# Kernel optimization log

Measured on AMD Instinct MI355X. Metric: run time of the kernel, lower is better.

Reference implementation:

```python
import jax, jax.numpy as jnp
import numpy as np

D_MODEL = 1024
N_HEADS = 16
HEAD_DIM = D_MODEL // N_HEADS


def setup_inputs() -> dict:
    key = jax.random.key(0)
    ks = jax.random.split(key, 5)
    T, B = 2048, 2
    x = jax.random.normal(ks[0], (T, B, D_MODEL), dtype=jnp.float32)
    s = 1.0 / np.sqrt(D_MODEL)
    Wq = jax.random.normal(ks[1], (D_MODEL, D_MODEL), dtype=jnp.float32) * s
    Wk = jax.random.normal(ks[2], (D_MODEL, D_MODEL), dtype=jnp.float32) * s
    Wv = jax.random.normal(ks[3], (D_MODEL, D_MODEL), dtype=jnp.float32) * s
    Wo = jax.random.normal(ks[4], (D_MODEL, D_MODEL), dtype=jnp.float32) * s
    return {"x": x, "Wq": Wq, "Wk": Wk, "Wv": Wv, "Wo": Wo}


def reference(x, Wq, Wk, Wv, Wo):
    T, B, C = x.shape
    H, D = N_HEADS, HEAD_DIM

    def split_heads(t):
        # (T,B,C) -> (B,H,T,D), matching view+permute(1,2,0,3)
        return t.reshape(T, B, H, D).transpose(1, 2, 0, 3)

    q = split_heads(x @ Wq.T)
    k = split_heads(x @ Wk.T)
    v = split_heads(x @ Wv.T)

    scale = 1.0 / jnp.sqrt(jnp.asarray(D, dtype=x.dtype))
    scores = jnp.einsum('bhqd,bhkd->bhqk', q, k) * scale  # (B,H,T,T)
    causal = jnp.tril(jnp.ones((T, T), dtype=bool))
    scores = jnp.where(causal, scores, jnp.asarray(-jnp.inf, dtype=scores.dtype))
    probs = jax.nn.softmax(scores, axis=-1)
    ctx = jnp.einsum('bhqk,bhkd->bhqd', probs, v)  # (B,H,T,D)
    ctx = ctx.transpose(2, 0, 1, 3).reshape(T, B, C)
    return ctx @ Wo.T
```

## Files before the change

### kernel.cpp

```cpp
#include <hip/hip_runtime.h>
#include <hip/hip_bf16.h>

#define TT 2048
#define BB 2
#define CC 1024
#define HH 16
#define DD 64
#define MM (TT * BB)

typedef short bf16x8 __attribute__((ext_vector_type(8)));
typedef float f32x4  __attribute__((ext_vector_type(4)));

__device__ inline ushort f2b(float f) {
    union { float f; unsigned u; } v; v.f = f;
    unsigned r = v.u + 0x7FFFu + ((v.u >> 16) & 1u);
    return (ushort)(r >> 16);
}

__device__ inline unsigned pack_bf16(float a, float b) {
    __hip_bfloat162 h = __float22bfloat162_rn(make_float2(a, b));
    union { __hip_bfloat162 h; unsigned u; } c; c.h = h;
    return c.u;
}

__device__ inline void gload_lds16(const ushort* g, ushort* l) {
    __builtin_amdgcn_global_load_lds(
        (const __attribute__((address_space(1))) void*)g,
        (__attribute__((address_space(3))) void*)l, 16, 0, 0);
}

#define XQUADS (MM * CC / 4)
#define WQUADS (CC * CC / 4)
__global__ __launch_bounds__(256) void conv_all(const float* __restrict__ x,
                                                const float* __restrict__ Wq,
                                                const float* __restrict__ Wk,
                                                const float* __restrict__ Wv,
                                                const float* __restrict__ Wo,
                                                ushort* __restrict__ dst) {
    int idx = blockIdx.x * 256 + threadIdx.x;
    const float* src;
    int off;
    if (idx < XQUADS) {
        src = x; off = idx;
    } else {
        int wi = (idx - XQUADS) >> 18;
        off = (idx - XQUADS) & (WQUADS - 1);
        src = (wi == 0) ? Wq : (wi == 1) ? Wk : (wi == 2) ? Wv : Wo;
    }
    float4 v = ((const float4*)src)[off];
    ushort4 o = {f2b(v.x), f2b(v.y), f2b(v.z), f2b(v.w)};
    ((ushort4*)dst)[idx] = o;
}

__global__ __launch_bounds__(256) void gemm_qkv(const ushort* __restrict__ A,
                                                const ushort* __restrict__ B0,
                                                const ushort* __restrict__ B1,
                                                const ushort* __restrict__ B2,
                                                ushort* __restrict__ Oq,
                                                ushort* __restrict__ Ok,
                                                ushort* __restrict__ Ov) {
    __shared__ __align__(16) ushort As[128 * 32];
    __shared__ __align__(16) ushort Bs[128 * 32];

    const int tid = threadIdx.x;
    const int wave = tid >> 6, lane = tid & 63;
    const int quad = lane >> 4, l16 = lane & 15;
    const int wm = wave >> 1, wn = wave & 1;

    const int bm = blockIdx.x * 128;
    const int by = blockIdx.y;
    const int wsel = by >> 3;
    const ushort* Bp = (wsel == 0) ? B0 : (wsel == 1) ? B1 : B2;
    const int bn = (by & 7) * 128;

    const int srow = lane >> 2;
    const int scol = (lane & 3) * 8;

    f32x4 acc[4][4];
#pragma unroll
    for (int i = 0; i < 4; i++)
#pragma unroll
        for (int j = 0; j < 4; j++) acc[i][j] = (f32x4){0.f, 0.f, 0.f, 0.f};

    for (int k0 = 0; k0 < CC; k0 += 32) {
#pragma unroll
        for (int i = 0; i < 2; i++) {
            const int rbase = wave * 32 + i * 16;
            gload_lds16(A + (size_t)(bm + rbase + srow) * CC + k0 + scol,
                        As + rbase * 32);
            gload_lds16(Bp + (size_t)(bn + rbase + srow) * CC + k0 + scol,
                        Bs + rbase * 32);
        }
        __syncthreads();

        bf16x8 af[4], bf[4];
#pragma unroll
        for (int mi = 0; mi < 4; mi++)
            af[mi] = *(const bf16x8*)(As + (wm * 64 + mi * 16 + l16) * 32 + quad * 8);
#pragma unroll
        for (int ni = 0; ni < 4; ni++)
            bf[ni] = *(const bf16x8*)(Bs + (wn * 64 + ni * 16 + l16) * 32 + quad * 8);
#pragma unroll
        for (int mi = 0; mi < 4; mi++)
#pragma unroll
            for (int ni = 0; ni < 4; ni++)
                acc[mi][ni] = __builtin_amdgcn_mfma_f32_16x16x32_bf16(
                    af[mi], bf[ni], acc[mi][ni], 0, 0, 0);
        __syncthreads();
    }

#pragma unroll
    for (int mi = 0; mi < 4; mi++) {
#pragma unroll
        for (int r = 0; r < 4; r++) {
            const int m = bm + wm * 64 + mi * 16 + quad * 4 + r;
#pragma unroll
            for (int ni = 0; ni < 4; ni++) {
                const int colg = bn + wn * 64 + ni * 16 + l16;
                float v = acc[mi][ni][r];
                if (wsel == 0) v *= 0.18033688f;
                const int t = m >> 1, b = m & 1;
                const int h = colg >> 6, d = colg & 63;
                ushort* dst = (wsel == 0) ? Oq : (wsel == 1) ? Ok : Ov;
                dst[(((size_t)(b * HH + h)) * TT + t) * DD + d] = f2b(v);
            }
        }
    }
}

__global__ __launch_bounds__(256) void gemm_out(const ushort* __restrict__ A,
                                                const ushort* __restrict__ Bm,
                                                float* __restrict__ Of) {
    __shared__ __align__(16) ushort As[128 * 32];
    __shared__ __align__(16) ushort Bs[64 * 32];

    const int tid = threadIdx.x;
    const int wave = tid >> 6, lane = tid & 63;
    const int quad = lane >> 4, l16 = lane & 15;

    const int bm = blockIdx.x * 128;
    const int bn = blockIdx.y * 64;

    const int srow = lane >> 2;
    const int scol = (lane & 3) * 8;

    f32x4 acc[2][4];
#pragma unroll
    for (int i = 0; i < 2; i++)
#pragma unroll
        for (int j = 0; j < 4; j++) acc[i][j] = (f32x4){0.f, 0.f, 0.f, 0.f};

    for (int k0 = 0; k0 < CC; k0 += 32) {
#pragma unroll
        for (int i = 0; i < 2; i++) {
            const int rbase = wave * 32 + i * 16;
            gload_lds16(A + (size_t)(bm + rbase + srow) * CC + k0 + scol,
                        As + rbase * 32);
        }
        gload_lds16(Bm + (size_t)(bn + wave * 16 + srow) * CC + k0 + scol,
                    Bs + wave * 16 * 32);
        __syncthreads();

        bf16x8 af[2], bf[4];
#pragma unroll
        for (int mi = 0; mi < 2; mi++)
            af[mi] = *(const bf16x8*)(As + (wave * 32 + mi * 16 + l16) * 32 + quad * 8);
#pragma unroll
        for (int ni = 0; ni < 4; ni++)
            bf[ni] = *(const bf16x8*)(Bs + (ni * 16 + l16) * 32 + quad * 8);
#pragma unroll
        for (int mi = 0; mi < 2; mi++)
#pragma unroll
            for (int ni = 0; ni < 4; ni++)
                acc[mi][ni] = __builtin_amdgcn_mfma_f32_16x16x32_bf16(
                    af[mi], bf[ni], acc[mi][ni], 0, 0, 0);
        __syncthreads();
    }

#pragma unroll
    for (int mi = 0; mi < 2; mi++)
#pragma unroll
        for (int r = 0; r < 4; r++) {
            const int m = bm + wave * 32 + mi * 16 + quad * 4 + r;
#pragma unroll
            for (int ni = 0; ni < 4; ni++)
                Of[(size_t)m * CC + bn + ni * 16 + l16] = acc[mi][ni][r];
        }
}

__global__ __launch_bounds__(256) void prep_kv(const ushort* __restrict__ Kb,
                                               const ushort* __restrict__ Vb,
                                               ushort* __restrict__ Kf,
                                               ushort* __restrict__ Vf) {
    __shared__ __align__(16) ushort Ls[64 * 72];
    const int tile = blockIdx.x;
    const int bh   = blockIdx.y;
    const int t    = threadIdx.x;
    const size_t src = (size_t)bh * TT * DD + (size_t)tile * 64 * DD;
    const size_t dst = (size_t)bh * TT * DD + (size_t)tile * 4096;

#pragma unroll
    for (int i = 0; i < 2; i++) {
        int e = t + i * 256;
        int r = e >> 3, kc = (e & 7) * 8;
        *(uint4*)(Ls + r * 72 + kc) = *(const uint4*)(Kb + src + r * 64 + kc);
    }
    __syncthreads();
#pragma unroll
    for (int i = 0; i < 2; i++) {
        int o = t + i * 256;
        int c = o >> 8, nb = (o >> 6) & 3, lane = o & 63;
        int quad = lane >> 4, l16 = lane & 15;
        int j = nb * 16 + l16, k0 = c * 32 + quad * 8;
        *(uint4*)(Kf + dst + (size_t)o * 8) = *(const uint4*)(Ls + j * 72 + k0);
    }
    __syncthreads();

#pragma unroll
    for (int i = 0; i < 2; i++) {
        int e = t + i * 256;
        int r = e >> 3, kc = (e & 7) * 8;
        *(uint4*)(Ls + r * 72 + kc) = *(const uint4*)(Vb + src + r * 64 + kc);
    }
    __syncthreads();
#pragma unroll
    for (int i = 0; i < 2; i++) {
        int o = t + i * 256;
        int c = o >> 8, db = (o >> 6) & 3, lane = o & 63;
        int quad = lane >> 4, l16 = lane & 15;
        int d = db * 16 + l16;
        ushort tmp[8];
#pragma unroll
        for (int u = 0; u < 8; u++) {
            int jp = c * 32 + quad * 8 + u;
            int j = (jp & 3) * 16 + (jp >> 2);
            tmp[u] = Ls[j * 72 + d];
        }
        *(uint4*)(Vf + dst + (size_t)o * 8) = *(uint4*)tmp;
    }
}

template <bool DIAG>
__device__ __forceinline__ void attn_step(const bf16x8* qa, f32x4* O, float* l,
                                          const bf16x8* kf, const bf16x8* vf,
                                          ushort* P, int j0, int qbase,
                                          int quad, int l16) {
    f32x4 S[4];
#pragma unroll
    for (int nb = 0; nb < 4; nb++) S[nb] = (f32x4){0.f, 0.f, 0.f, 0.f};
#pragma unroll
    for (int c = 0; c < 2; c++)
#pragma unroll
        for (int nb = 0; nb < 4; nb++)
            S[nb] = __builtin_amdgcn_mfma_f32_16x16x32_bf16(qa[c], kf[c * 4 + nb],
                                                            S[nb], 0, 0, 0);

#pragma unroll
    for (int r = 0; r < 4; r++) {
        const int qg = qbase + quad * 4 + r;
        float p[4];
#pragma unroll
        for (int nb = 0; nb < 4; nb++) {
            float s = S[nb][r];
            if (DIAG) { if (j0 + nb * 16 + l16 > qg) s = -1e30f; }
            p[nb] = __builtin_amdgcn_exp2f(s);
        }
        l[r] += (p[0] + p[1]) + (p[2] + p[3]);
        uint2 w; w.x = pack_bf16(p[0], p[1]); w.y = pack_bf16(p[2], p[3]);
        *(uint2*)(P + (quad * 4 + r) * 72 + l16 * 4) = w;
    }

#pragma unroll
    for (int c = 0; c < 2; c++) {
        bf16x8 pa = *(const bf16x8*)(P + l16 * 72 + c * 32 + quad * 8);
#pragma unroll
        for (int db = 0; db < 4; db++)
            O[db] = __builtin_amdgcn_mfma_f32_16x16x32_bf16(pa, vf[c * 4 + db],
                                                            O[db], 0, 0, 0);
    }
}

__global__ __launch_bounds__(256, 2) void attn_mfma(const ushort* __restrict__ Qb,
                                                    const ushort* __restrict__ Kf,
                                                    const ushort* __restrict__ Vf,
                                                    ushort* __restrict__ ctx) {
    __shared__ __align__(16) ushort PsA[4 * 16 * 72];
    __shared__ __align__(16) ushort PsB[4 * 16 * 72];

    const int tid  = threadIdx.x;
    const int wave = tid >> 6;
    const int lane = tid & 63;
    const int quad = lane >> 4;
    const int l16  = lane & 15;

    const int p  = blockIdx.x;
    const int bh = blockIdx.y;
    const int qtA = p, qtB = (TT / 64 - 1) - p;
    const int q0A = qtA * 64 + wave * 16;
    const int q0B = qtB * 64 + wave * 16;

    const size_t baseQK = (size_t)bh * TT * DD;

    bf16x8 qaA[2], qaB[2];
    {
        const ushort* qp = Qb + baseQK + (size_t)(q0A + l16) * DD + quad * 8;
        qaA[0] = *(const bf16x8*)(qp);
        qaA[1] = *(const bf16x8*)(qp + 32);
        const ushort* qp2 = Qb + baseQK + (size_t)(q0B + l16) * DD + quad * 8;
        qaB[0] = *(const bf16x8*)(qp2);
        qaB[1] = *(const bf16x8*)(qp2 + 32);
    }

    f32x4 OA[4], OB[4];
#pragma unroll
    for (int i = 0; i < 4; i++) {
        OA[i] = (f32x4){0.f, 0.f, 0.f, 0.f};
        OB[i] = (f32x4){0.f, 0.f, 0.f, 0.f};
    }
    float lA[4] = {0.f, 0.f, 0.f, 0.f};
    float lB[4] = {0.f, 0.f, 0.f, 0.f};

    ushort* PA = PsA + wave * 16 * 72;
    ushort* PB = PsB + wave * 16 * 72;

    const ushort* Kfp = Kf + baseQK;
    const ushort* Vfp = Vf + baseQK;

    for (int kt = 0; kt <= qtB; kt++) {
        const int j0 = kt * 64;

        bf16x8 kf[8], vf[8];
#pragma unroll
        for (int i = 0; i < 8; i++) {
            kf[i] = *(const bf16x8*)(Kfp + (i << 9) + lane * 8);
            vf[i] = *(const bf16x8*)(Vfp + (i << 9) + lane * 8);
        }

        if (kt == qtB)
            attn_step<true >(qaB, OB, lB, kf, vf, PB, j0, q0B, quad, l16);
        else
            attn_step<false>(qaB, OB, lB, kf, vf, PB, j0, q0B, quad, l16);

        if (kt < qtA)
            attn_step<false>(qaA, OA, lA, kf, vf, PA, j0, q0A, quad, l16);
        else if (kt == qtA)
            attn_step<true >(qaA, OA, lA, kf, vf, PA, j0, q0A, quad, l16);

        Kfp += 4096;
        Vfp += 4096;
    }

    const int b = bh >> 4, h = bh & 15;
#pragma unroll
    for (int r = 0; r < 4; r++) {
        float la = lA[r], lb = lB[r];
        la += __shfl_xor(la, 1); la += __shfl_xor(la, 2);
        la += __shfl_xor(la, 4); la += __shfl_xor(la, 8);
        lb += __shfl_xor(lb, 1); lb += __shfl_xor(lb, 2);
        lb += __shfl_xor(lb, 4); lb += __shfl_xor(lb, 8);
        const float invA = 1.f / la;
        const float invB = 1.f / lb;
        const int tA = q0A + quad * 4 + r;
        const int tB = q0B + quad * 4 + r;
#pragma unroll
        for (int db = 0; db < 4; db++) {
            ctx[((size_t)tA * BB + b) * CC + h * DD + db * 16 + l16] =
                f2b(OA[db][r] * invA);
            ctx[((size_t)tB * BB + b) * CC + h * DD + db * 16 + l16] =
                f2b(OB[db][r] * invB);
        }
    }
}

extern "C" void kernel_launch(void* const* d_in, const int* in_sizes, int n_in,
                              void* d_out, int out_size, void* d_ws, size_t ws_size,
                              hipStream_t stream) {
    const float* x  = (const float*)d_in[0];
    const float* Wq = (const float*)d_in[1];
    const float* Wk = (const float*)d_in[2];
    const float* Wv = (const float*)d_in[3];
    const float* Wo = (const float*)d_in[4];
    float* out = (float*)d_out;

    ushort* xb  = (ushort*)d_ws;
    ushort* Wb  = xb + (size_t)MM * CC;
    ushort* Wqb = Wb;
    ushort* Wkb = Wb + (size_t)CC * CC;
    ushort* Wvb = Wb + 2 * (size_t)CC * CC;
    ushort* Wob = Wb + 3 * (size_t)CC * CC;
    ushort* Qb  = Wb + 4 * (size_t)CC * CC;
    ushort* Kb  = Qb + (size_t)MM * CC;
    ushort* Vb  = Kb + (size_t)MM * CC;
    ushort* Kf  = Vb + (size_t)MM * CC;
    ushort* Vf  = Kf + (size_t)MM * CC;
    ushort* Ctxb = Vf + (size_t)MM * CC;

    conv_all<<<dim3((XQUADS + 4 * WQUADS) / 256), 256, 0, stream>>>(
        x, Wq, Wk, Wv, Wo, xb);

    gemm_qkv<<<dim3(MM / 128, 24), 256, 0, stream>>>(
        xb, Wqb, Wkb, Wvb, Qb, Kb, Vb);

    prep_kv<<<dim3(TT / 64, BB * HH), 256, 0, stream>>>(Kb, Vb, Kf, Vf);

    attn_mfma<<<dim3(TT / 128, BB * HH), 256, 0, stream>>>(Qb, Kf, Vf, Ctxb);

    gemm_out<<<dim3(MM / 128, CC / 64), 256, 0, stream>>>(Ctxb, Wob, out);
}
```

Baseline: 176.2 us.

## Write K in attention fragment layout from QKV GEMM and prefetch K/V tiles

The QKV GEMM epilogue now writes K straight into the MFMA-fragment layout that the attention kernel consumes. This removes the K half of the separate prep kernel, leaving a V-only prep_v, and saves one intermediate buffer plus a read/write pass. The attention loop also loads the next K/V tile into registers while the current tile is computed, to hide global-load latency. The extra register buffers may raise VGPR pressure and lower occupancy.

```diff
diff --git a/kernel.cpp b/kernel.cpp
--- a/kernel.cpp
+++ b/kernel.cpp
@@ -118,11 +118,21 @@
             for (int ni = 0; ni < 4; ni++) {
                 const int colg = bn + wn * 64 + ni * 16 + l16;
                 float v = acc[mi][ni][r];
-                if (wsel == 0) v *= 0.18033688f;
                 const int t = m >> 1, b = m & 1;
                 const int h = colg >> 6, d = colg & 63;
-                ushort* dst = (wsel == 0) ? Oq : (wsel == 1) ? Ok : Ov;
-                dst[(((size_t)(b * HH + h)) * TT + t) * DD + d] = f2b(v);
+                if (wsel == 0) {
+                    v *= 0.18033688f;
+                    Oq[(((size_t)(b * HH + h)) * TT + t) * DD + d] = f2b(v);
+                } else if (wsel == 1) {
+                    const int jj = t & 63;
+                    size_t idx = ((size_t)(b * HH + h) * TT) * DD
+                               + (size_t)(t >> 6) * 4096
+                               + (d >> 5) * 2048 + (jj >> 4) * 512
+                               + (((d >> 3) & 3) * 16 + (jj & 15)) * 8 + (d & 7);
+                    Ok[idx] = f2b(v);
+                } else {
+                    Ov[(((size_t)(b * HH + h)) * TT + t) * DD + d] = f2b(v);
+                }
             }
         }
     }
@@ -188,33 +198,14 @@
         }
 }
 
-__global__ __launch_bounds__(256) void prep_kv(const ushort* __restrict__ Kb,
-                                               const ushort* __restrict__ Vb,
-                                               ushort* __restrict__ Kf,
-                                               ushort* __restrict__ Vf) {
+__global__ __launch_bounds__(256) void prep_v(const ushort* __restrict__ Vb,
+                                              ushort* __restrict__ Vf) {
     __shared__ __align__(16) ushort Ls[64 * 72];
     const int tile = blockIdx.x;
     const int bh   = blockIdx.y;
     const int t    = threadIdx.x;
     const size_t src = (size_t)bh * TT * DD + (size_t)tile * 64 * DD;
     const size_t dst = (size_t)bh * TT * DD + (size_t)tile * 4096;
-
-#pragma unroll
-    for (int i = 0; i < 2; i++) {
-        int e = t + i * 256;
-        int r = e >> 3, kc = (e & 7) * 8;
-        *(uint4*)(Ls + r * 72 + kc) = *(const uint4*)(Kb + src + r * 64 + kc);
-    }
-    __syncthreads();
-#pragma unroll
-    for (int i = 0; i < 2; i++) {
-        int o = t + i * 256;
-        int c = o >> 8, nb = (o >> 6) & 3, lane = o & 63;
-        int quad = lane >> 4, l16 = lane & 15;
-        int j = nb * 16 + l16, k0 = c * 32 + quad * 8;
-        *(uint4*)(Kf + dst + (size_t)o * 8) = *(const uint4*)(Ls + j * 72 + k0);
-    }
-    __syncthreads();
 
 #pragma unroll
     for (int i = 0; i < 2; i++) {
@@ -326,14 +317,24 @@
     const ushort* Kfp = Kf + baseQK;
     const ushort* Vfp = Vf + baseQK;
 
+    bf16x8 kf[8], vf[8], kn[8], vn[8];
+#pragma unroll
+    for (int i = 0; i < 8; i++) {
+        kf[i] = *(const bf16x8*)(Kfp + (i << 9) + lane * 8);
+        vf[i] = *(const bf16x8*)(Vfp + (i << 9) + lane * 8);
+    }
+
     for (int kt = 0; kt <= qtB; kt++) {
         const int j0 = kt * 64;
 
-        bf16x8 kf[8], vf[8];
-#pragma unroll
-        for (int i = 0; i < 8; i++) {
-            kf[i] = *(const bf16x8*)(Kfp + (i << 9) + lane * 8);
-            vf[i] = *(const bf16x8*)(Vfp + (i << 9) + lane * 8);
+        if (kt < qtB) {
+            const ushort* Kn = Kfp + (((size_t)kt + 1) << 12);
+            const ushort* Vn = Vfp + (((size_t)kt + 1) << 12);
+#pragma unroll
+            for (int i = 0; i < 8; i++) {
+                kn[i] = *(const bf16x8*)(Kn + (i << 9) + lane * 8);
+                vn[i] = *(const bf16x8*)(Vn + (i << 9) + lane * 8);
+            }
         }
 
         if (kt == qtB)
@@ -346,8 +347,8 @@
         else if (kt == qtA)
             attn_step<true >(qaA, OA, lA, kf, vf, PA, j0, q0A, quad, l16);
 
-        Kfp += 4096;
-        Vfp += 4096;
+#pragma unroll
+        for (int i = 0; i < 8; i++) { kf[i] = kn[i]; vf[i] = vn[i]; }
     }
 
     const int b = bh >> 4, h = bh & 15;
@@ -389,21 +390,20 @@
     ushort* Wvb = Wb + 2 * (size_t)CC * CC;
     ushort* Wob = Wb + 3 * (size_t)CC * CC;
     ushort* Qb  = Wb + 4 * (size_t)CC * CC;
-    ushort* Kb  = Qb + (size_t)MM * CC;
-    ushort* Vb  = Kb + (size_t)MM * CC;
-    ushort* Kf  = Vb + (size_t)MM * CC;
-    ushort* Vf  = Kf + (size_t)MM * CC;
+    ushort* Kf  = Qb + (size_t)MM * CC;
+    ushort* Vb  = Kf + (size_t)MM * CC;
+    ushort* Vf  = Vb + (size_t)MM * CC;
     ushort* Ctxb = Vf + (size_t)MM * CC;
 
     conv_all<<<dim3((XQUADS + 4 * WQUADS) / 256), 256, 0, stream>>>(
         x, Wq, Wk, Wv, Wo, xb);
 
     gemm_qkv<<<dim3(MM / 128, 24), 256, 0, stream>>>(
-        xb, Wqb, Wkb, Wvb, Qb, Kb, Vb);
-
-    prep_kv<<<dim3(TT / 64, BB * HH), 256, 0, stream>>>(Kb, Vb, Kf, Vf);
-
-    attn_mfma<<<dim3(TT / 128, BB * HH), 256, 0, stream>>>(Qb, Kf, Vf, Ctxb);
+        xb, Wqb, Wkb, Wvb, Qb, Kf, Vb);
+
+    prep_v<<<dim3(TT / 64, BB * HH), 256, 0, stream>>>(Vb, Vf);
+
+    attn_mfma<<<dim3(16, BB * HH), 256, 0, stream>>>(Qb, Kf, Vf, Ctxb);
 
     gemm_out<<<dim3(MM / 128, CC / 64), 256, 0, stream>>>(Ctxb, Wob, out);
 }
```

Measured after the change: 181.4 us. +3.0%, slower.
